# Kernel optimization log

Measured on AMD Instinct MI355X. Metric: run time of the kernel, lower is better.

## Reference

```python
import jax, jax.numpy as jnp
import numpy as np

B, Q, K, D, H = 16, 128, 128, 512, 512
NEG = -1e6


def setup_inputs() -> dict:
    key = jax.random.key(0)
    ks = jax.random.split(key, 7)
    return {
        "queries": jax.random.normal(ks[0], (B, Q, D), dtype=jnp.float32),
        "keys": jax.random.normal(ks[1], (B, K, D), dtype=jnp.float32),
        "values": jax.random.normal(ks[2], (B, K, D), dtype=jnp.float32),
        "valid_lens": jax.random.randint(ks[3], (B,), 1, K + 1, dtype=jnp.int32),
        "Wq": jax.random.normal(ks[4], (D, H), dtype=jnp.float32) / np.sqrt(D),
        "Wk": jax.random.normal(ks[5], (D, H), dtype=jnp.float32) / np.sqrt(D),
        "wv": jax.random.normal(ks[6], (H,), dtype=jnp.float32) / np.sqrt(H),
    }


def reference(queries, keys, values, valid_lens, Wq, Wk, wv):
    # projections (LazyLinear, bias=False)
    q = jnp.einsum("bqd,dh->bqh", queries, Wq)  # [B,Q,H]
    k = jnp.einsum("bkd,dh->bkh", keys, Wk)    # [B,K,H]
    # broadcast add -> tanh -> reduce to scalar score (Bahdanau)
    feats = jnp.tanh(q[:, :, None, :] + k[:, None, :, :])  # [B,Q,K,H]
    scores = jnp.einsum("bqkh,h->bqk", feats, wv)           # [B,Q,K]
    # masked softmax over key dim using per-batch valid lengths
    mask = jnp.arange(scores.shape[-1])[None, None, :] < valid_lens[:, None, None]
    scores = jnp.where(mask, scores, NEG)
    attn = jax.nn.softmax(scores, axis=-1)                  # [B,Q,K]
    # dropout is identity in eval mode
    return jnp.einsum("bqk,bkv->bqv", attn, values)
```

## Files before the change

### kernel.cpp

```cpp
#include <hip/hip_runtime.h>

#define Bn 16
#define Qn 128
#define Kn 128
#define Dn 512
#define Hn 512
#define NEGV (-3.0e38f)
#define PSCALE 2.8853900817779268f

typedef short s16x8 __attribute__((ext_vector_type(8)));
typedef float f32x4 __attribute__((ext_vector_type(4)));

__device__ __forceinline__ float exp2_hw(float x) {
  float r;
  asm("v_exp_f32 %0, %1" : "=v"(r) : "v"(x));
  return r;
}
__device__ __forceinline__ float rcp_hw(float x) { return __builtin_amdgcn_rcpf(x); }
__device__ __forceinline__ unsigned short f2bf(float f) {
  unsigned int u = __float_as_uint(f);
  u += 0x7fff + ((u >> 16) & 1);
  return (unsigned short)(u >> 16);
}

__global__ __launch_bounds__(256) void convert_w(
    const float* __restrict__ Wq, const float* __restrict__ Wk,
    unsigned short* __restrict__ Wt)
{
  const int tid = blockIdx.x * 256 + threadIdx.x;
  const int n = tid & 511, rest = tid >> 9;
  const int sel = rest >> 5, k16 = rest & 31;
  const float* W = sel ? Wk : Wq;
  unsigned short o[16];
  #pragma unroll
  for (int i = 0; i < 16; ++i)
    o[i] = f2bf(W[(size_t)(k16 * 16 + i) * Hn + n]);
  unsigned short* dst = Wt + (size_t)sel * 262144 + (size_t)n * 512 + k16 * 16;
  #pragma unroll
  for (int j = 0; j < 4; ++j) *(ushort4*)(dst + j * 4) = *(ushort4*)&o[j * 4];
}

__global__ __launch_bounds__(256) void proj_mfma(
    const float* __restrict__ queries, const float* __restrict__ keys,
    const unsigned short* __restrict__ Wt, const float* __restrict__ wv,
    float* __restrict__ QW, float* __restrict__ Ekq)
{
  __shared__ unsigned short Al[64][72];
  __shared__ unsigned short Bl[128][72];
  __shared__ float Tep[64][68];
  const int t = threadIdx.x, w = t >> 6, l = t & 63;
  const int wm = w >> 1, wn = w & 1;
  const int rowTile = blockIdx.x;
  const int n0 = blockIdx.y * 128;
  const int R0 = rowTile * 64;
  const bool isQ = rowTile < 32;
  const float* Asrc = isQ ? queries : keys;
  const int rowBase = isQ ? R0 : (R0 - 2048);
  const unsigned short* Wsel = Wt + (isQ ? 0 : 262144);

  f32x4 acc[2][4];
  #pragma unroll
  for (int m = 0; m < 2; ++m)
    #pragma unroll
    for (int n = 0; n < 4; ++n) acc[m][n] = (f32x4)0.f;

  const int lr = l & 15, lk = l >> 4;

  for (int k0 = 0; k0 < Hn; k0 += 64) {
    float4 afr[4];
    ushort4 br[4][2];
    #pragma unroll
    for (int i = 0; i < 4; ++i) {
      int g = t + 256 * i, r = g >> 4, c4 = g & 15;
      afr[i] = *(const float4*)(Asrc + (size_t)(rowBase + r) * Dn + k0 + c4 * 4);
    }
    #pragma unroll
    for (int i = 0; i < 4; ++i) {
      int g = t + 256 * i, r = g >> 3, c = g & 7;
      const unsigned short* p = Wsel + (size_t)(n0 + r) * Hn + k0 + c * 8;
      br[i][0] = *(const ushort4*)p; br[i][1] = *(const ushort4*)(p + 4);
    }
    __syncthreads();
    #pragma unroll
    for (int i = 0; i < 4; ++i) {
      int g = t + 256 * i, r = g >> 4, c4 = g & 15;
      ushort4 o = {f2bf(afr[i].x), f2bf(afr[i].y), f2bf(afr[i].z), f2bf(afr[i].w)};
      *(ushort4*)&Al[r][c4 * 4] = o;
    }
    #pragma unroll
    for (int i = 0; i < 4; ++i) {
      int g = t + 256 * i, r = g >> 3, c = g & 7;
      *(ushort4*)&Bl[r][c * 8] = br[i][0]; *(ushort4*)&Bl[r][c * 8 + 4] = br[i][1];
    }
    __syncthreads();
    #pragma unroll
    for (int ks = 0; ks < 2; ++ks) {
      s16x8 af[2], bf_[4];
      #pragma unroll
      for (int m = 0; m < 2; ++m)
        af[m] = *(const s16x8*)&Al[wm * 32 + m * 16 + lr][ks * 32 + lk * 8];
      #pragma unroll
      for (int n = 0; n < 4; ++n)
        bf_[n] = *(const s16x8*)&Bl[wn * 64 + n * 16 + lr][ks * 32 + lk * 8];
      #pragma unroll
      for (int m = 0; m < 2; ++m)
        #pragma unroll
        for (int n = 0; n < 4; ++n)
          acc[m][n] = __builtin_amdgcn_mfma_f32_16x16x32_bf16(af[m], bf_[n], acc[m][n], 0, 0, 0);
    }
    __syncthreads();
  }

  if (isQ) {
    #pragma unroll
    for (int m = 0; m < 2; ++m)
      #pragma unroll
      for (int n = 0; n < 4; ++n)
        #pragma unroll
        for (int r = 0; r < 4; ++r) {
          int row = R0 + wm * 32 + m * 16 + lk * 4 + r;
          int col = n0 + wn * 64 + n * 16 + lr;
          float a = acc[m][n][r];
          float F  = exp2_hw(-PSCALE * a);
          float WF = -2.f * wv[col] * F;
          float2 o = {WF, F};
          *(float2*)(QW + ((size_t)row * Hn + col) * 2) = o;
        }
  } else {
    const int krow0 = R0 - 2048;
    const int bb = krow0 >> 7, kb = krow0 & 127;
    const int hl = t >> 2, kq = (t & 3) * 16;
    #pragma unroll
    for (int hc = 0; hc < 2; ++hc) {
      __syncthreads();
      if (wn == hc) {
        #pragma unroll
        for (int m = 0; m < 2; ++m)
          #pragma unroll
          for (int n = 0; n < 4; ++n)
            #pragma unroll
            for (int r = 0; r < 4; ++r) {
              int row_l = wm * 32 + m * 16 + lk * 4 + r;
              int h_l = n * 16 + lr;
              Tep[h_l][row_l] = exp2_hw(PSCALE * acc[m][n][r]);
            }
      }
      __syncthreads();
      float* dst = Ekq + (size_t)bb * 65536 + (size_t)(n0 + hc * 64 + hl) * 128 + kb + kq;
      #pragma unroll
      for (int j = 0; j < 4; ++j)
        *(float4*)(dst + j * 4) = *(const float4*)&Tep[hl][kq + j * 4];
    }
  }
}

__global__ __launch_bounds__(256) void score_kernel(
    const float* __restrict__ QW, const float* __restrict__ Ekq,
    float* __restrict__ Sp)
{
  __shared__ float EkL[8192];
  __shared__ float QWL[32][132];
  const int id = blockIdx.x;
  const int g = id & 127, qt = id >> 7;
  const int b = g >> 3, hs = g & 7;
  const int t = threadIdx.x, w = t >> 6, l = t & 63;
  const int qp = w * 8 + ((l >> 4) << 1);
  const int ka = (l & 15) * 4;
  const int h0 = hs * 64;

  {
    const float4* esrc = (const float4*)(Ekq + (size_t)b * 65536 + (size_t)hs * 8192);
    float4 er[8];
    #pragma unroll
    for (int i = 0; i < 8; ++i) er[i] = esrc[t + 256 * i];
    const float* qsrc = QW + ((size_t)(b * Qn + qt * 32) * Hn + h0) * 2;
    const int qrow = t >> 3, qc = (t & 7) * 16;
    float4 qr4[4];
    #pragma unroll
    for (int i = 0; i < 4; ++i)
      qr4[i] = *(const float4*)(qsrc + (size_t)qrow * 1024 + qc + i * 4);
    float4* edst = (float4*)EkL;
    #pragma unroll
    for (int i = 0; i < 8; ++i) edst[t + 256 * i] = er[i];
    #pragma unroll
    for (int i = 0; i < 4; ++i)
      *(float4*)&QWL[qrow][qc + i * 4] = qr4[i];
  }
  __syncthreads();

  float acc0[8], acc1[8];
  #pragma unroll
  for (int j = 0; j < 8; ++j) { acc0[j] = 0.f; acc1[j] = 0.f; }

  #pragma unroll 4
  for (int hb = 0; hb < 32; ++hb) {
    const float* ekp = EkL + hb * 256;
    float4 ea0 = *(const float4*)(ekp + ka);
    float4 ea1 = *(const float4*)(ekp + 64 + ka);
    float4 eb0 = *(const float4*)(ekp + 128 + ka);
    float4 eb1 = *(const float4*)(ekp + 192 + ka);
    float4 qv0 = *(const float4*)&QWL[qp][hb * 4];
    float4 qv1 = *(const float4*)&QWL[qp + 1][hb * 4];
    {
      const float WF0 = qv0.x, F0 = qv0.y, WF1 = qv0.z, F1 = qv0.w;
      float d0, d1, num;
      d0 = F0 + ea0.x; d1 = F1 + eb0.x;
      num = __builtin_fmaf(WF0, d1, WF1 * d0);
      acc0[0] = __builtin_fmaf(num, rcp_hw(d0 * d1), acc0[0]);
      d0 = F0 + ea0.y; d1 = F1 + eb0.y;
      num = __builtin_fmaf(WF0, d1, WF1 * d0);
      acc0[1] = __builtin_fmaf(num, rcp_hw(d0 * d1), acc0[1]);
      d0 = F0 + ea0.z; d1 = F1 + eb0.z;
      num = __builtin_fmaf(WF0, d1, WF1 * d0);
      acc0[2] = __builtin_fmaf(num, rcp_hw(d0 * d1), acc0[2]);
      d0 = F0 + ea0.w; d1 = F1 + eb0.w;
      num = __builtin_fmaf(WF0, d1, WF1 * d0);
      acc0[3] = __builtin_fmaf(num, rcp_hw(d0 * d1), acc0[3]);
      d0 = F0 + ea1.x; d1 = F1 + eb1.x;
      num = __builtin_fmaf(WF0, d1, WF1 * d0);
      acc0[4] = __builtin_fmaf(num, rcp_hw(d0 * d1), acc0[4]);
      d0 = F0 + ea1.y; d1 = F1 + eb1.y;
      num = __builtin_fmaf(WF0, d1, WF1 * d0);
      acc0[5] = __builtin_fmaf(num, rcp_hw(d0 * d1), acc0[5]);
      d0 = F0 + ea1.z; d1 = F1 + eb1.z;
      num = __builtin_fmaf(WF0, d1, WF1 * d0);
      acc0[6] = __builtin_fmaf(num, rcp_hw(d0 * d1), acc0[6]);
      d0 = F0 + ea1.w; d1 = F1 + eb1.w;
      num = __builtin_fmaf(WF0, d1, WF1 * d0);
      acc0[7] = __builtin_fmaf(num, rcp_hw(d0 * d1), acc0[7]);
    }
    {
      const float WF0 = qv1.x, F0 = qv1.y, WF1 = qv1.z, F1 = qv1.w;
      float d0, d1, num;
      d0 = F0 + ea0.x; d1 = F1 + eb0.x;
      num = __builtin_fmaf(WF0, d1, WF1 * d0);
      acc1[0] = __builtin_fmaf(num, rcp_hw(d0 * d1), acc1[0]);
      d0 = F0 + ea0.y; d1 = F1 + eb0.y;
      num = __builtin_fmaf(WF0, d1, WF1 * d0);
      acc1[1] = __builtin_fmaf(num, rcp_hw(d0 * d1), acc1[1]);
      d0 = F0 + ea0.z; d1 = F1 + eb0.z;
      num = __builtin_fmaf(WF0, d1, WF1 * d0);
      acc1[2] = __builtin_fmaf(num, rcp_hw(d0 * d1), acc1[2]);
      d0 = F0 + ea0.w; d1 = F1 + eb0.w;
      num = __builtin_fmaf(WF0, d1, WF1 * d0);
      acc1[3] = __builtin_fmaf(num, rcp_hw(d0 * d1), acc1[3]);
      d0 = F0 + ea1.x; d1 = F1 + eb1.x;
      num = __builtin_fmaf(WF0, d1, WF1 * d0);
      acc1[4] = __builtin_fmaf(num, rcp_hw(d0 * d1), acc1[4]);
      d0 = F0 + ea1.y; d1 = F1 + eb1.y;
      num = __builtin_fmaf(WF0, d1, WF1 * d0);
      acc1[5] = __builtin_fmaf(num, rcp_hw(d0 * d1), acc1[5]);
      d0 = F0 + ea1.z; d1 = F1 + eb1.z;
      num = __builtin_fmaf(WF0, d1, WF1 * d0);
      acc1[6] = __builtin_fmaf(num, rcp_hw(d0 * d1), acc1[6]);
      d0 = F0 + ea1.w; d1 = F1 + eb1.w;
      num = __builtin_fmaf(WF0, d1, WF1 * d0);
      acc1[7] = __builtin_fmaf(num, rcp_hw(d0 * d1), acc1[7]);
    }
  }

  const int q = qt * 32 + qp;
  size_t sb = (((size_t)hs * Bn + b) * Qn + q) * Kn;
  *(float4*)(Sp + sb + ka)            = (float4){acc0[0], acc0[1], acc0[2], acc0[3]};
  *(float4*)(Sp + sb + 64 + ka)       = (float4){acc0[4], acc0[5], acc0[6], acc0[7]};
  *(float4*)(Sp + sb + Kn + ka)       = (float4){acc1[0], acc1[1], acc1[2], acc1[3]};
  *(float4*)(Sp + sb + Kn + 64 + ka)  = (float4){acc1[4], acc1[5], acc1[6], acc1[7]};
}

__global__ __launch_bounds__(512) void softmax_kernel(
    const float* __restrict__ Sp, const int* __restrict__ valid_lens,
    unsigned short* __restrict__ At)
{
  const int t = threadIdx.x;
  const int b = blockIdx.y;
  const int q = blockIdx.x * 16 + (t >> 5);
  const int k0 = (t & 31) * 4;
  const size_t base = ((size_t)b * Qn + q) * Kn + k0;

  float s[4] = {0.f, 0.f, 0.f, 0.f};
  #pragma unroll
  for (int p = 0; p < 8; ++p) {
    float4 sv = *(const float4*)(Sp + base + (size_t)p * 262144);
    s[0] += sv.x; s[1] += sv.y; s[2] += sv.z; s[3] += sv.w;
  }

  const int vlen = valid_lens[b];
  bool ok[4];
  float m = NEGV;
  #pragma unroll
  for (int j = 0; j < 4; ++j) {
    ok[j] = (k0 + j) < vlen;
    if (ok[j]) m = fmaxf(m, s[j]);
  }
  #pragma unroll
  for (int xm = 16; xm >= 1; xm >>= 1) m = fmaxf(m, __shfl_xor(m, xm, 32));
  float e[4], sum = 0.f;
  #pragma unroll
  for (int j = 0; j < 4; ++j) {
    e[j] = ok[j] ? exp2_hw((s[j] - m) * 1.44269504f) : 0.f;
    sum += e[j];
  }
  #pragma unroll
  for (int xm = 16; xm >= 1; xm >>= 1) sum += __shfl_xor(sum, xm, 32);
  float inv = rcp_hw(sum);
  ushort4 o = {f2bf(e[0] * inv), f2bf(e[1] * inv), f2bf(e[2] * inv), f2bf(e[3] * inv)};
  *(ushort4*)(At + base) = o;
}

__global__ __launch_bounds__(256) void av_mfma(
    const unsigned short* __restrict__ At, const float* __restrict__ values,
    float* __restrict__ out)
{
  __shared__ unsigned short AtL[128][72];
  __shared__ unsigned short VL[64][72];
  const int t = threadIdx.x, w = t >> 6, l = t & 63;
  const int wm = w >> 1, wn = w & 1;
  const int dt = blockIdx.x;
  const int b = blockIdx.y;
  const int lr = l & 15, lk = l >> 4;

  f32x4 acc[4][2];
  #pragma unroll
  for (int m = 0; m < 4; ++m)
    #pragma unroll
    for (int n = 0; n < 2; ++n) acc[m][n] = (f32x4)0.f;

  const unsigned short* Atb = At + (size_t)b * Qn * Kn;

  for (int k0 = 0; k0 < Kn; k0 += 64) {
    ushort4 ar[4][2];
    float4 vv[4];
    #pragma unroll
    for (int i = 0; i < 4; ++i) {
      int g = t + 256 * i, r = g >> 3, c = g & 7;
      const unsigned short* p = Atb + (size_t)r * Kn + k0 + c * 8;
      ar[i][0] = *(const ushort4*)p; ar[i][1] = *(const ushort4*)(p + 4);
    }
    #pragma unroll
    for (int j = 0; j < 4; ++j) {
      int idx = t + 256 * j, k_l = idx >> 4, d4 = idx & 15;
      vv[j] = *(const float4*)(values + ((size_t)(b * Kn) + k0 + k_l) * Dn + dt * 64 + d4 * 4);
    }
    __syncthreads();
    #pragma unroll
    for (int i = 0; i < 4; ++i) {
      int g = t + 256 * i, r = g >> 3, c = g & 7;
      *(ushort4*)&AtL[r][c * 8] = ar[i][0]; *(ushort4*)&AtL[r][c * 8 + 4] = ar[i][1];
    }
    #pragma unroll
    for (int j = 0; j < 4; ++j) {
      int idx = t + 256 * j, k_l = idx >> 4, d4 = idx & 15;
      VL[d4 * 4 + 0][k_l] = f2bf(vv[j].x);
      VL[d4 * 4 + 1][k_l] = f2bf(vv[j].y);
      VL[d4 * 4 + 2][k_l] = f2bf(vv[j].z);
      VL[d4 * 4 + 3][k_l] = f2bf(vv[j].w);
    }
    __syncthreads();
    #pragma unroll
    for (int ks = 0; ks < 2; ++ks) {
      s16x8 af[4], bf_[2];
      #pragma unroll
      for (int m = 0; m < 4; ++m)
        af[m] = *(const s16x8*)&AtL[wm * 64 + m * 16 + lr][ks * 32 + lk * 8];
      #pragma unroll
      for (int n = 0; n < 2; ++n)
        bf_[n] = *(const s16x8*)&VL[wn * 32 + n * 16 + lr][ks * 32 + lk * 8];
      #pragma unroll
      for (int m = 0; m < 4; ++m)
        #pragma unroll
        for (int n = 0; n < 2; ++n)
          acc[m][n] = __builtin_amdgcn_mfma_f32_16x16x32_bf16(af[m], bf_[n], acc[m][n], 0, 0, 0);
    }
    __syncthreads();
  }

  #pragma unroll
  for (int m = 0; m < 4; ++m)
    #pragma unroll
    for (int n = 0; n < 2; ++n)
      #pragma unroll
      for (int r = 0; r < 4; ++r) {
        int row = wm * 64 + m * 16 + lk * 4 + r;
        int col = dt * 64 + wn * 32 + n * 16 + lr;
        out[((size_t)(b * Qn) + row) * Dn + col] = acc[m][n][r];
      }
}

extern "C" void kernel_launch(void* const* d_in, const int* in_sizes, int n_in,
                              void* d_out, int out_size, void* d_ws, size_t ws_size,
                              hipStream_t stream) {
  const float* queries    = (const float*)d_in[0];
  const float* keys       = (const float*)d_in[1];
  const float* values     = (const float*)d_in[2];
  const int*   valid_lens = (const int*)d_in[3];
  const float* Wq         = (const float*)d_in[4];
  const float* Wk         = (const float*)d_in[5];
  const float* wv         = (const float*)d_in[6];
  float* out = (float*)d_out;

  unsigned short* Wt  = (unsigned short*)d_ws;
  float*          QW  = (float*)(Wt + 524288);
  float*          Ekq = QW + 2097152;
  float*          Sp  = Ekq + 1048576;
  unsigned short* At  = (unsigned short*)(Sp + 2097152);

  convert_w<<<128, 256, 0, stream>>>(Wq, Wk, Wt);
  proj_mfma<<<dim3(64, 4), 256, 0, stream>>>(queries, keys, Wt, wv, QW, Ekq);
  score_kernel<<<512, 256, 0, stream>>>(QW, Ekq, Sp);
  softmax_kernel<<<dim3(8, 16), 512, 0, stream>>>(Sp, valid_lens, At);
  av_mfma<<<dim3(8, 16), 256, 0, stream>>>(At, values, out);
}
```

Before: 49.04 us.

## Fuse masked softmax into attention-times-values MFMA kernel

Merges the softmax kernel and the attn@values GEMM into one kernel. Each block computes softmax for 16 query rows straight into shared memory as bf16, then loops over all 512 output columns, staging bf16-converted values tiles in LDS and running MFMA. This removes one launch and the global round trip of the attention matrix. In exchange, each block re-reads and re-converts the full values slab for its batch (8x redundant across query tiles), and each block now covers only 16 query rows, which gives less MFMA work per tile load.

```diff
diff --git a/kernel.cpp b/kernel.cpp
--- a/kernel.cpp
+++ b/kernel.cpp
@@ -21,6 +21,9 @@
   unsigned int u = __float_as_uint(f);
   u += 0x7fff + ((u >> 16) & 1);
   return (unsigned short)(u >> 16);
+}
+__device__ __forceinline__ unsigned int pack2bf(float lo, float hi) {
+  return (unsigned int)f2bf(lo) | ((unsigned int)f2bf(hi) << 16);
 }
 
 __global__ __launch_bounds__(256) void convert_w(
@@ -267,123 +270,92 @@
   *(float4*)(Sp + sb + Kn + 64 + ka)  = (float4){acc1[4], acc1[5], acc1[6], acc1[7]};
 }
 
-__global__ __launch_bounds__(512) void softmax_kernel(
+__global__ __launch_bounds__(256) void softmax_av(
     const float* __restrict__ Sp, const int* __restrict__ valid_lens,
-    unsigned short* __restrict__ At)
+    const float* __restrict__ values, float* __restrict__ out)
 {
-  const int t = threadIdx.x;
-  const int b = blockIdx.y;
-  const int q = blockIdx.x * 16 + (t >> 5);
-  const int k0 = (t & 31) * 4;
-  const size_t base = ((size_t)b * Qn + q) * Kn + k0;
-
-  float s[4] = {0.f, 0.f, 0.f, 0.f};
-  #pragma unroll
-  for (int p = 0; p < 8; ++p) {
-    float4 sv = *(const float4*)(Sp + base + (size_t)p * 262144);
-    s[0] += sv.x; s[1] += sv.y; s[2] += sv.z; s[3] += sv.w;
-  }
-
-  const int vlen = valid_lens[b];
-  bool ok[4];
-  float m = NEGV;
-  #pragma unroll
-  for (int j = 0; j < 4; ++j) {
-    ok[j] = (k0 + j) < vlen;
-    if (ok[j]) m = fmaxf(m, s[j]);
-  }
-  #pragma unroll
-  for (int xm = 16; xm >= 1; xm >>= 1) m = fmaxf(m, __shfl_xor(m, xm, 32));
-  float e[4], sum = 0.f;
-  #pragma unroll
-  for (int j = 0; j < 4; ++j) {
-    e[j] = ok[j] ? exp2_hw((s[j] - m) * 1.44269504f) : 0.f;
-    sum += e[j];
-  }
-  #pragma unroll
-  for (int xm = 16; xm >= 1; xm >>= 1) sum += __shfl_xor(sum, xm, 32);
-  float inv = rcp_hw(sum);
-  ushort4 o = {f2bf(e[0] * inv), f2bf(e[1] * inv), f2bf(e[2] * inv), f2bf(e[3] * inv)};
-  *(ushort4*)(At + base) = o;
-}
-
-__global__ __launch_bounds__(256) void av_mfma(
-    const unsigned short* __restrict__ At, const float* __restrict__ values,
-    float* __restrict__ out)
-{
-  __shared__ unsigned short AtL[128][72];
-  __shared__ unsigned short VL[64][72];
+  __shared__ unsigned short AtL[16][136];
+  __shared__ unsigned int VLu[128][36];
   const int t = threadIdx.x, w = t >> 6, l = t & 63;
-  const int wm = w >> 1, wn = w & 1;
-  const int dt = blockIdx.x;
-  const int b = blockIdx.y;
+  const int b = blockIdx.y, qt = blockIdx.x;
   const int lr = l & 15, lk = l >> 4;
 
-  f32x4 acc[4][2];
-  #pragma unroll
-  for (int m = 0; m < 4; ++m)
-    #pragma unroll
-    for (int n = 0; n < 2; ++n) acc[m][n] = (f32x4)0.f;
-
-  const unsigned short* Atb = At + (size_t)b * Qn * Kn;
-
-  for (int k0 = 0; k0 < Kn; k0 += 64) {
-    ushort4 ar[4][2];
-    float4 vv[4];
-    #pragma unroll
-    for (int i = 0; i < 4; ++i) {
-      int g = t + 256 * i, r = g >> 3, c = g & 7;
-      const unsigned short* p = Atb + (size_t)r * Kn + k0 + c * 8;
-      ar[i][0] = *(const ushort4*)p; ar[i][1] = *(const ushort4*)(p + 4);
-    }
-    #pragma unroll
-    for (int j = 0; j < 4; ++j) {
-      int idx = t + 256 * j, k_l = idx >> 4, d4 = idx & 15;
-      vv[j] = *(const float4*)(values + ((size_t)(b * Kn) + k0 + k_l) * Dn + dt * 64 + d4 * 4);
-    }
-    __syncthreads();
-    #pragma unroll
-    for (int i = 0; i < 4; ++i) {
-      int g = t + 256 * i, r = g >> 3, c = g & 7;
-      *(ushort4*)&AtL[r][c * 8] = ar[i][0]; *(ushort4*)&AtL[r][c * 8 + 4] = ar[i][1];
-    }
-    #pragma unroll
-    for (int j = 0; j < 4; ++j) {
-      int idx = t + 256 * j, k_l = idx >> 4, d4 = idx & 15;
-      VL[d4 * 4 + 0][k_l] = f2bf(vv[j].x);
-      VL[d4 * 4 + 1][k_l] = f2bf(vv[j].y);
-      VL[d4 * 4 + 2][k_l] = f2bf(vv[j].z);
-      VL[d4 * 4 + 3][k_l] = f2bf(vv[j].w);
-    }
-    __syncthreads();
-    #pragma unroll
-    for (int ks = 0; ks < 2; ++ks) {
-      s16x8 af[4], bf_[2];
-      #pragma unroll
-      for (int m = 0; m < 4; ++m)
-        af[m] = *(const s16x8*)&AtL[wm * 64 + m * 16 + lr][ks * 32 + lk * 8];
-      #pragma unroll
-      for (int n = 0; n < 2; ++n)
-        bf_[n] = *(const s16x8*)&VL[wn * 32 + n * 16 + lr][ks * 32 + lk * 8];
-      #pragma unroll
-      for (int m = 0; m < 4; ++m)
+  {
+    const int q_l = t >> 4, k8 = (t & 15) * 8;
+    const size_t base = ((size_t)(b * Qn) + qt * 16 + q_l) * Kn + k8;
+    float s[8] = {0.f, 0.f, 0.f, 0.f, 0.f, 0.f, 0.f, 0.f};
+    #pragma unroll
+    for (int p = 0; p < 8; ++p) {
+      float4 a0 = *(const float4*)(Sp + base + (size_t)p * 262144);
+      float4 a1 = *(const float4*)(Sp + base + (size_t)p * 262144 + 4);
+      s[0] += a0.x; s[1] += a0.y; s[2] += a0.z; s[3] += a0.w;
+      s[4] += a1.x; s[5] += a1.y; s[6] += a1.z; s[7] += a1.w;
+    }
+    const int vlen = valid_lens[b];
+    bool ok[8];
+    float m = NEGV;
+    #pragma unroll
+    for (int j = 0; j < 8; ++j) {
+      ok[j] = (k8 + j) < vlen;
+      if (ok[j]) m = fmaxf(m, s[j]);
+    }
+    #pragma unroll
+    for (int xm = 8; xm >= 1; xm >>= 1) m = fmaxf(m, __shfl_xor(m, xm));
+    float e[8], sum = 0.f;
+    #pragma unroll
+    for (int j = 0; j < 8; ++j) {
+      e[j] = ok[j] ? exp2_hw((s[j] - m) * 1.44269504f) : 0.f;
+      sum += e[j];
+    }
+    #pragma unroll
+    for (int xm = 8; xm >= 1; xm >>= 1) sum += __shfl_xor(sum, xm);
+    float inv = rcp_hw(sum);
+    ushort4 o0 = {f2bf(e[0] * inv), f2bf(e[1] * inv), f2bf(e[2] * inv), f2bf(e[3] * inv)};
+    ushort4 o1 = {f2bf(e[4] * inv), f2bf(e[5] * inv), f2bf(e[6] * inv), f2bf(e[7] * inv)};
+    *(ushort4*)&AtL[q_l][k8] = o0;
+    *(ushort4*)&AtL[q_l][k8 + 4] = o1;
+  }
+
+  const int kread = t & 15, dread = (t >> 4) & 15;
+  #pragma unroll
+  for (int dt = 0; dt < 4; ++dt) {
+    f32x4 acc[2];
+    acc[0] = (f32x4)0.f; acc[1] = (f32x4)0.f;
+    #pragma unroll
+    for (int k0 = 0; k0 < Kn; k0 += 64) {
+      __syncthreads();
+      #pragma unroll
+      for (int j = 0; j < 4; ++j) {
+        int k2 = kread + 16 * (j & 1);
+        int d4 = dread + 16 * (j >> 1);
+        const float* vp = values + ((size_t)(b * Kn) + k0 + 2 * k2) * Dn + dt * 128 + d4 * 4;
+        float4 v0 = *(const float4*)(vp);
+        float4 v1 = *(const float4*)(vp + Dn);
+        VLu[d4 * 4 + 0][k2] = pack2bf(v0.x, v1.x);
+        VLu[d4 * 4 + 1][k2] = pack2bf(v0.y, v1.y);
+        VLu[d4 * 4 + 2][k2] = pack2bf(v0.z, v1.z);
+        VLu[d4 * 4 + 3][k2] = pack2bf(v0.w, v1.w);
+      }
+      __syncthreads();
+      #pragma unroll
+      for (int ks = 0; ks < 2; ++ks) {
+        s16x8 af = *(const s16x8*)&AtL[lr][k0 + ks * 32 + lk * 8];
         #pragma unroll
-        for (int n = 0; n < 2; ++n)
-          acc[m][n] = __builtin_amdgcn_mfma_f32_16x16x32_bf16(af[m], bf_[n], acc[m][n], 0, 0, 0);
-    }
-    __syncthreads();
-  }
-
-  #pragma unroll
-  for (int m = 0; m < 4; ++m)
-    #pragma unroll
-    for (int n = 0; n < 2; ++n)
+        for (int nn = 0; nn < 2; ++nn) {
+          s16x8 bv = *(const s16x8*)&VLu[w * 32 + nn * 16 + lr][ks * 16 + lk * 4];
+          acc[nn] = __builtin_amdgcn_mfma_f32_16x16x32_bf16(af, bv, acc[nn], 0, 0, 0);
+        }
+      }
+    }
+    #pragma unroll
+    for (int nn = 0; nn < 2; ++nn)
       #pragma unroll
       for (int r = 0; r < 4; ++r) {
-        int row = wm * 64 + m * 16 + lk * 4 + r;
-        int col = dt * 64 + wn * 32 + n * 16 + lr;
-        out[((size_t)(b * Qn) + row) * Dn + col] = acc[m][n][r];
+        int q = qt * 16 + lk * 4 + r;
+        int d = dt * 128 + w * 32 + nn * 16 + lr;
+        out[((size_t)(b * Qn) + q) * Dn + d] = acc[nn][r];
       }
+  }
 }
 
 extern "C" void kernel_launch(void* const* d_in, const int* in_sizes, int n_in,
@@ -402,11 +374,9 @@
   float*          QW  = (float*)(Wt + 524288);
   float*          Ekq = QW + 2097152;
   float*          Sp  = Ekq + 1048576;
-  unsigned short* At  = (unsigned short*)(Sp + 2097152);
 
   convert_w<<<128, 256, 0, stream>>>(Wq, Wk, Wt);
   proj_mfma<<<dim3(64, 4), 256, 0, stream>>>(queries, keys, Wt, wv, QW, Ekq);
   score_kernel<<<512, 256, 0, stream>>>(QW, Ekq, Sp);
-  softmax_kernel<<<dim3(8, 16), 512, 0, stream>>>(Sp, valid_lens, At);
-  av_mfma<<<dim3(8, 16), 256, 0, stream>>>(At, values, out);
-}
+  softmax_av<<<dim3(8, 16), 256, 0, stream>>>(Sp, valid_lens, values, out);
+}
```

Result: slower. 55.19 us (+12.5%).
